# Kernel optimization log

Hardware: AMD Instinct MI355X
Metric: run time of the kernel (lower is better)

The kernel has to match this reference:

```python
import itertools
import jax, jax.numpy as jnp
import numpy as np

KERNEL = (2, 2)
NIN = 4            # prod(KERNEL)
NPAT = 16          # 2 ** NIN
# Faithful to the torch code: every kernel offset shifts dim 0 (the transposes
# swap dims 1 and d+1 and never touch dim 0), so each flattened kernel slot is a
# roll of x along axis 0 by -(sum of offsets), row-major over kernel indices.
SHIFTS = tuple(sum(idx) for idx in itertools.product(*(range(k) for k in KERNEL)))
BITS = np.asarray(list(itertools.product((0, 1), repeat=NIN)), dtype=np.float32)  # (NPAT, NIN)


def setup_inputs() -> dict:
    key = jax.random.key(0)
    k1, k2 = jax.random.split(key)
    x = jax.random.uniform(k1, (256, 64, 64), dtype=jnp.float32)                 # inputs in [0,1)
    toggle_gates = jax.random.uniform(k2, (4, NPAT, 64, 64), dtype=jnp.float32)  # torch.rand init
    return {"x": x, "toggle_gates": toggle_gates}


def _convolve(v):
    # (B,H,W) -> (B,H,W,NIN): shifted neighbor stack (rolls along dim 0, as in the torch code)
    return jnp.stack([jnp.roll(v, -s, axis=0) for s in SHIFTS], axis=-1)


def _pattern_weights(conv):
    # weight[b,h,w,p] = prod_j (conv_j if bit_j(p) else 1-conv_j)
    # equals prod_j (1 - |bit_j(p) - conv_j|) since bits are 0/1
    bits = jnp.asarray(BITS)  # (NPAT, NIN)
    w = jnp.ones(conv.shape[:-1] + (NPAT,), conv.dtype)
    for j in range(NIN):  # NIN=4, small fixed loop
        vj = conv[..., j:j + 1]  # (B,H,W,1)
        w = w * (vj * bits[:, j] + (1.0 - vj) * (1.0 - bits[:, j]))
    return w  # (B,H,W,NPAT)


def reference(x, toggle_gates):
    layers = toggle_gates.shape[0]
    tw = jax.nn.sigmoid(toggle_gates)  # (L,NPAT,H,W)
    outputs = x
    reg = jnp.asarray(0.0, x.dtype)
    for i in range(layers):
        conv = _convolve(outputs)          # (B,H,W,NIN)
        w = _pattern_weights(conv)         # (B,H,W,NPAT)
        if i:
            reg = reg - (jnp.mean(jnp.log(w)) + jnp.mean(jnp.log(1.0 - w)))
        # (weight * toggle).sum over pattern axis
        outputs = jnp.clip(jnp.einsum('bhwp,phw->bhw', w, tw[i]), 0.0, 1.0)
    return outputs, reg / (layers - 1)
```

## Files before the change

### kernel.cpp

```cpp
#include <hip/hip_runtime.h>

#define BATCH 256
#define HWSZ  4096
#define COLS  16
#define BSTR  17

__global__ __launch_bounds__(256) void fused_kernel(
    const float* __restrict__ x,
    const float* __restrict__ tg,
    float* __restrict__ out,
    float* __restrict__ partials)
{
    __shared__ float bufA[BATCH * BSTR];
    __shared__ float bufB[BATCH * BSTR];
    __shared__ float tws[64 * COLS];
    __shared__ float wsum[4];

    const int tid  = threadIdx.x;
    const int hw0  = blockIdx.x * COLS;
    const int c    = tid & 15;
    const int brow = tid >> 4;
    const int b0   = brow * 16;

#pragma unroll
    for (int k = 0; k < 4; ++k) {
        int idx = tid + k * 256;
        int c2 = idx & 15;
        int lp = idx >> 4;
        float g = tg[lp * HWSZ + hw0 + c2];
        tws[lp * COLS + c2] = 1.0f / (1.0f + __expf(-g));
    }

#pragma unroll
    for (int k = 0; k < 16; ++k) {
        int idx = tid + k * 256;
        int b = idx >> 4;
        int c2 = idx & 15;
        bufA[b * BSTR + c2] = x[b * HWSZ + hw0 + c2];
    }

    float racc = 0.0f;
    float* src = bufA;
    float* dst = bufB;

#pragma unroll
    for (int l = 0; l < 4; ++l) {
        __syncthreads();

        const float* tl = &tws[l * 16 * COLS + c];
        float T0  = tl[0 * COLS], T1 = tl[1 * COLS];
        float T24 = tl[2 * COLS] + tl[4 * COLS];
        float T35 = tl[3 * COLS] + tl[5 * COLS];
        float T6  = tl[6 * COLS], T7 = tl[7 * COLS];
        float T8  = tl[8 * COLS], T9 = tl[9 * COLS];
        float TAC = tl[10 * COLS] + tl[12 * COLS];
        float TBD = tl[11 * COLS] + tl[13 * COLS];
        float TE  = tl[14 * COLS], TF = tl[15 * COLS];

        float v0 = src[b0 * BSTR + c];
        float v1 = src[(b0 + 1) * BSTR + c];

#pragma unroll
        for (int k = 0; k < 16; ++k) {
            float v2 = src[((b0 + k + 2) & 255) * BSTR + c];
            float a0 = 1.0f - v0, a1 = 1.0f - v1, a2 = 1.0f - v2;

            float g0 = a1 * a1, g1 = a1 * v1, g2 = v1 * v1;
            float u00 = a0 * g0, u01 = a0 * g1, u02 = a0 * g2;
            float u10 = v0 * g0, u11 = v0 * g1, u12 = v0 * g2;

            float w0 = u00 * a2, w1 = u00 * v2;
            float w2 = u01 * a2, w3 = u01 * v2;
            float w6 = u02 * a2, w7 = u02 * v2;
            float w8 = u10 * a2, w9 = u10 * v2;
            float wA = u11 * a2, wB = u11 * v2;
            float wE = u12 * a2, wF = u12 * v2;

            float acc = w0 * T0 + w1 * T1 + w2 * T24 + w3 * T35
                      + w6 * T6 + w7 * T7 + w8 * T8 + w9 * T9
                      + wA * TAC + wB * TBD + wE * TE + wF * TF;
            float o = fminf(fmaxf(acc, 0.0f), 1.0f);

            if (l == 3) out[(b0 + k) * HWSZ + hw0 + c] = o;
            else        dst[(b0 + k) * BSTR + c] = o;

            if (l >= 1) {
                float s1 = (1.0f - w0) * (1.0f - w1) * (1.0f - w6) * (1.0f - w7)
                         * (1.0f - w8) * (1.0f - w9) * (1.0f - wE) * (1.0f - wF);
                float s2 = (1.0f - w2) * (1.0f - w3) * (1.0f - wA) * (1.0f - wB);
                float pB = s1 * s2 * s2;
                float pA = (v0 * a0) * (g1 * g1) * (v2 * a2);
                racc += 8.0f * __logf(pA) + __logf(pB);
            }
            v0 = v1; v1 = v2;
        }
        float* t = src; src = dst; dst = t;
    }

#pragma unroll
    for (int off = 32; off; off >>= 1) racc += __shfl_down(racc, off, 64);
    if ((tid & 63) == 0) wsum[tid >> 6] = racc;
    __syncthreads();
    if (tid == 0) partials[blockIdx.x] = wsum[0] + wsum[1] + wsum[2] + wsum[3];
}

__global__ void finalize_kernel(const float* __restrict__ partials,
                                float* __restrict__ out_reg)
{
    int tid = threadIdx.x;
    double v = (double)partials[tid];
#pragma unroll
    for (int off = 32; off; off >>= 1) v += __shfl_down(v, off, 64);
    __shared__ double ws[4];
    if ((tid & 63) == 0) ws[tid >> 6] = v;
    __syncthreads();
    if (tid == 0) {
        double tot = ws[0] + ws[1] + ws[2] + ws[3];
        out_reg[0] = (float)(-tot / (16777216.0 * 3.0));
    }
}

extern "C" void kernel_launch(void* const* d_in, const int* in_sizes, int n_in,
                              void* d_out, int out_size, void* d_ws, size_t ws_size,
                              hipStream_t stream)
{
    const float* x  = (const float*)d_in[0];
    const float* tg = (const float*)d_in[1];
    float* out      = (float*)d_out;
    float* partials = (float*)d_ws;

    fused_kernel<<<dim3(HWSZ / COLS), dim3(256), 0, stream>>>(x, tg, out, partials);
    finalize_kernel<<<1, 256, 0, stream>>>(partials, out + (size_t)BATCH * HWSZ);
}
```

Measured before the change: 72.48 us.

## Split batch across blocks with halo recompute to raise occupancy

Adds a second grid dimension that splits the batch into 64-row chunks. Each block loads an 8-row halo and recomputes the overlapping rows at each layer so the four layers still fuse without communicating between blocks. This shrinks shared memory per block and quadruples the block count, meant to fix low occupancy (256 blocks, ~35KB LDS each). The cost is redundant halo computation, extra loads, and four times as many partial sums for the finalize kernel.

After: 74.50 us. 1.03x slower.

```diff
diff --git a/kernel.cpp b/kernel.cpp
--- a/kernel.cpp
+++ b/kernel.cpp
@@ -4,23 +4,25 @@
 #define HWSZ  4096
 #define COLS  16
 #define BSTR  17
+#define CB    64
+#define XROWS (CB + 8)
 
-__global__ __launch_bounds__(256) void fused_kernel(
+__global__ __launch_bounds__(256, 4) void fused_kernel(
     const float* __restrict__ x,
     const float* __restrict__ tg,
     float* __restrict__ out,
     float* __restrict__ partials)
 {
-    __shared__ float bufA[BATCH * BSTR];
-    __shared__ float bufB[BATCH * BSTR];
+    __shared__ float bufA[XROWS * BSTR];
+    __shared__ float bufB[XROWS * BSTR];
     __shared__ float tws[64 * COLS];
     __shared__ float wsum[4];
 
-    const int tid  = threadIdx.x;
-    const int hw0  = blockIdx.x * COLS;
-    const int c    = tid & 15;
-    const int brow = tid >> 4;
-    const int b0   = brow * 16;
+    const int tid = threadIdx.x;
+    const int hw0 = blockIdx.x * COLS;
+    const int b0  = blockIdx.y * CB;
+    const int c   = tid & 15;
+    const int r   = tid >> 4;
 
 #pragma unroll
     for (int k = 0; k < 4; ++k) {
@@ -32,11 +34,13 @@
     }
 
 #pragma unroll
-    for (int k = 0; k < 16; ++k) {
+    for (int k = 0; k < 5; ++k) {
         int idx = tid + k * 256;
-        int b = idx >> 4;
-        int c2 = idx & 15;
-        bufA[b * BSTR + c2] = x[b * HWSZ + hw0 + c2];
+        if (idx < XROWS * COLS) {
+            int row = idx >> 4;
+            int c2  = idx & 15;
+            bufA[row * BSTR + c2] = x[((b0 + row) & 255) * HWSZ + hw0 + c2];
+        }
     }
 
     float racc = 0.0f;
@@ -45,6 +49,7 @@
 
 #pragma unroll
     for (int l = 0; l < 4; ++l) {
+        const int cnt = CB + 2 * (3 - l);
         __syncthreads();
 
         const float* tl = &tws[l * 16 * COLS + c];
@@ -57,42 +62,43 @@
         float TBD = tl[11 * COLS] + tl[13 * COLS];
         float TE  = tl[14 * COLS], TF = tl[15 * COLS];
 
-        float v0 = src[b0 * BSTR + c];
-        float v1 = src[(b0 + 1) * BSTR + c];
+#pragma unroll
+        for (int m = 0; m * 16 < CB + 2 * (3 - l); ++m) {
+            int idx = r + 16 * m;
+            if (idx < cnt) {
+                float v0 = src[idx * BSTR + c];
+                float v1 = src[(idx + 1) * BSTR + c];
+                float v2 = src[(idx + 2) * BSTR + c];
+                float a0 = 1.0f - v0, a1 = 1.0f - v1, a2 = 1.0f - v2;
 
-#pragma unroll
-        for (int k = 0; k < 16; ++k) {
-            float v2 = src[((b0 + k + 2) & 255) * BSTR + c];
-            float a0 = 1.0f - v0, a1 = 1.0f - v1, a2 = 1.0f - v2;
+                float g0 = a1 * a1, g1 = a1 * v1, g2 = v1 * v1;
+                float u00 = a0 * g0, u01 = a0 * g1, u02 = a0 * g2;
+                float u10 = v0 * g0, u11 = v0 * g1, u12 = v0 * g2;
 
-            float g0 = a1 * a1, g1 = a1 * v1, g2 = v1 * v1;
-            float u00 = a0 * g0, u01 = a0 * g1, u02 = a0 * g2;
-            float u10 = v0 * g0, u11 = v0 * g1, u12 = v0 * g2;
+                float w0 = u00 * a2, w1 = u00 * v2;
+                float w2 = u01 * a2, w3 = u01 * v2;
+                float w6 = u02 * a2, w7 = u02 * v2;
+                float w8 = u10 * a2, w9 = u10 * v2;
+                float wA = u11 * a2, wB = u11 * v2;
+                float wE = u12 * a2, wF = u12 * v2;
 
-            float w0 = u00 * a2, w1 = u00 * v2;
-            float w2 = u01 * a2, w3 = u01 * v2;
-            float w6 = u02 * a2, w7 = u02 * v2;
-            float w8 = u10 * a2, w9 = u10 * v2;
-            float wA = u11 * a2, wB = u11 * v2;
-            float wE = u12 * a2, wF = u12 * v2;
+                float acc = w0 * T0 + w1 * T1 + w2 * T24 + w3 * T35
+                          + w6 * T6 + w7 * T7 + w8 * T8 + w9 * T9
+                          + wA * TAC + wB * TBD + wE * TE + wF * TF;
+                float o = fminf(fmaxf(acc, 0.0f), 1.0f);
 
-            float acc = w0 * T0 + w1 * T1 + w2 * T24 + w3 * T35
-                      + w6 * T6 + w7 * T7 + w8 * T8 + w9 * T9
-                      + wA * TAC + wB * TBD + wE * TE + wF * TF;
-            float o = fminf(fmaxf(acc, 0.0f), 1.0f);
+                if (l == 3) out[(b0 + idx) * HWSZ + hw0 + c] = o;
+                else        dst[idx * BSTR + c] = o;
 
-            if (l == 3) out[(b0 + k) * HWSZ + hw0 + c] = o;
-            else        dst[(b0 + k) * BSTR + c] = o;
-
-            if (l >= 1) {
-                float s1 = (1.0f - w0) * (1.0f - w1) * (1.0f - w6) * (1.0f - w7)
-                         * (1.0f - w8) * (1.0f - w9) * (1.0f - wE) * (1.0f - wF);
-                float s2 = (1.0f - w2) * (1.0f - w3) * (1.0f - wA) * (1.0f - wB);
-                float pB = s1 * s2 * s2;
-                float pA = (v0 * a0) * (g1 * g1) * (v2 * a2);
-                racc += 8.0f * __logf(pA) + __logf(pB);
+                if (l >= 1 && idx < CB) {
+                    float s1 = (1.0f - w0) * (1.0f - w1) * (1.0f - w6) * (1.0f - w7)
+                             * (1.0f - w8) * (1.0f - w9) * (1.0f - wE) * (1.0f - wF);
+                    float s2 = (1.0f - w2) * (1.0f - w3) * (1.0f - wA) * (1.0f - wB);
+                    float pB = s1 * s2 * s2;
+                    float pA = (v0 * a0) * (g1 * g1) * (v2 * a2);
+                    racc += 8.0f * __logf(pA) + __logf(pB);
+                }
             }
-            v0 = v1; v1 = v2;
         }
         float* t = src; src = dst; dst = t;
     }
@@ -101,14 +107,18 @@
     for (int off = 32; off; off >>= 1) racc += __shfl_down(racc, off, 64);
     if ((tid & 63) == 0) wsum[tid >> 6] = racc;
     __syncthreads();
-    if (tid == 0) partials[blockIdx.x] = wsum[0] + wsum[1] + wsum[2] + wsum[3];
+    if (tid == 0)
+        partials[blockIdx.y * gridDim.x + blockIdx.x] =
+            wsum[0] + wsum[1] + wsum[2] + wsum[3];
 }
 
 __global__ void finalize_kernel(const float* __restrict__ partials,
                                 float* __restrict__ out_reg)
 {
     int tid = threadIdx.x;
-    double v = (double)partials[tid];
+    double v = 0.0;
+#pragma unroll
+    for (int k = 0; k < 4; ++k) v += (double)partials[tid + k * 256];
 #pragma unroll
     for (int off = 32; off; off >>= 1) v += __shfl_down(v, off, 64);
     __shared__ double ws[4];
@@ -129,6 +139,7 @@
     float* out      = (float*)d_out;
     float* partials = (float*)d_ws;
 
-    fused_kernel<<<dim3(HWSZ / COLS), dim3(256), 0, stream>>>(x, tg, out, partials);
+    fused_kernel<<<dim3(HWSZ / COLS, BATCH / CB), dim3(256), 0, stream>>>(
+        x, tg, out, partials);
     finalize_kernel<<<1, 256, 0, stream>>>(partials, out + (size_t)BATCH * HWSZ);
 }
```

## Hold batch rows in registers and pass neighbours by wave shuffles

Applied to the files above, without the earlier changes.

The kernel is restructured so each block handles 4 spatial columns with one wavefront per column. Each lane keeps 4 consecutive batch rows in registers and gets the next two rows from the neighbouring lane by shuffle, which replaces the per-layer shared-memory ping-pong buffers and the barriers between layers. This makes 1024 blocks with much less LDS each, raising occupancy, and loads and stores use float4 staged through a small shared transpose. The finalize kernel now sums 1024 partials.

Measured after the change: 76.00 us. 4.9% more time.

```diff
diff --git a/kernel.cpp b/kernel.cpp
--- a/kernel.cpp
+++ b/kernel.cpp
@@ -2,69 +2,59 @@
 
 #define BATCH 256
 #define HWSZ  4096
-#define COLS  16
-#define BSTR  17
 
-__global__ __launch_bounds__(256) void fused_kernel(
+__global__ __launch_bounds__(256, 4) void fused_kernel(
     const float* __restrict__ x,
     const float* __restrict__ tg,
     float* __restrict__ out,
     float* __restrict__ partials)
 {
-    __shared__ float bufA[BATCH * BSTR];
-    __shared__ float bufB[BATCH * BSTR];
-    __shared__ float tws[64 * COLS];
+    __shared__ float xs[BATCH * 5];
+    __shared__ float tws[256];
     __shared__ float wsum[4];
 
     const int tid  = threadIdx.x;
-    const int hw0  = blockIdx.x * COLS;
-    const int c    = tid & 15;
-    const int brow = tid >> 4;
-    const int b0   = brow * 16;
+    const int w    = tid >> 6;
+    const int lane = tid & 63;
+    const int nxt  = (lane + 1) & 63;
+    const int hw0  = blockIdx.x * 4;
 
-#pragma unroll
-    for (int k = 0; k < 4; ++k) {
-        int idx = tid + k * 256;
-        int c2 = idx & 15;
-        int lp = idx >> 4;
-        float g = tg[lp * HWSZ + hw0 + c2];
-        tws[lp * COLS + c2] = 1.0f / (1.0f + __expf(-g));
+    {
+        int lp = tid >> 2, cc = tid & 3;
+        float g = tg[lp * HWSZ + hw0 + cc];
+        tws[lp * 4 + cc] = 1.0f / (1.0f + __expf(-g));
     }
+    {
+        const float4 v = *reinterpret_cast<const float4*>(&x[tid * HWSZ + hw0]);
+        xs[tid * 5 + 0] = v.x; xs[tid * 5 + 1] = v.y;
+        xs[tid * 5 + 2] = v.z; xs[tid * 5 + 3] = v.w;
+    }
+    __syncthreads();
 
-#pragma unroll
-    for (int k = 0; k < 16; ++k) {
-        int idx = tid + k * 256;
-        int b = idx >> 4;
-        int c2 = idx & 15;
-        bufA[b * BSTR + c2] = x[b * HWSZ + hw0 + c2];
-    }
+    float cur0 = xs[(4 * lane + 0) * 5 + w];
+    float cur1 = xs[(4 * lane + 1) * 5 + w];
+    float cur2 = xs[(4 * lane + 2) * 5 + w];
+    float cur3 = xs[(4 * lane + 3) * 5 + w];
 
     float racc = 0.0f;
-    float* src = bufA;
-    float* dst = bufB;
 
 #pragma unroll
     for (int l = 0; l < 4; ++l) {
-        __syncthreads();
+        const float* tl = &tws[l * 64 + w];
+        float T0  = tl[0 * 4], T1 = tl[1 * 4];
+        float T24 = tl[2 * 4] + tl[4 * 4];
+        float T35 = tl[3 * 4] + tl[5 * 4];
+        float T6  = tl[6 * 4], T7 = tl[7 * 4];
+        float T8  = tl[8 * 4], T9 = tl[9 * 4];
+        float TAC = tl[10 * 4] + tl[12 * 4];
+        float TBD = tl[11 * 4] + tl[13 * 4];
+        float TE  = tl[14 * 4], TF = tl[15 * 4];
 
-        const float* tl = &tws[l * 16 * COLS + c];
-        float T0  = tl[0 * COLS], T1 = tl[1 * COLS];
-        float T24 = tl[2 * COLS] + tl[4 * COLS];
-        float T35 = tl[3 * COLS] + tl[5 * COLS];
-        float T6  = tl[6 * COLS], T7 = tl[7 * COLS];
-        float T8  = tl[8 * COLS], T9 = tl[9 * COLS];
-        float TAC = tl[10 * COLS] + tl[12 * COLS];
-        float TBD = tl[11 * COLS] + tl[13 * COLS];
-        float TE  = tl[14 * COLS], TF = tl[15 * COLS];
+        float e4 = __shfl(cur0, nxt, 64);
+        float e5 = __shfl(cur1, nxt, 64);
 
-        float v0 = src[b0 * BSTR + c];
-        float v1 = src[(b0 + 1) * BSTR + c];
-
-#pragma unroll
-        for (int k = 0; k < 16; ++k) {
-            float v2 = src[((b0 + k + 2) & 255) * BSTR + c];
+        auto elem = [&](float v0, float v1, float v2) -> float {
             float a0 = 1.0f - v0, a1 = 1.0f - v1, a2 = 1.0f - v2;
-
             float g0 = a1 * a1, g1 = a1 * v1, g2 = v1 * v1;
             float u00 = a0 * g0, u01 = a0 * g1, u02 = a0 * g2;
             float u10 = v0 * g0, u11 = v0 * g1, u12 = v0 * g2;
@@ -79,10 +69,6 @@
             float acc = w0 * T0 + w1 * T1 + w2 * T24 + w3 * T35
                       + w6 * T6 + w7 * T7 + w8 * T8 + w9 * T9
                       + wA * TAC + wB * TBD + wE * TE + wF * TF;
-            float o = fminf(fmaxf(acc, 0.0f), 1.0f);
-
-            if (l == 3) out[(b0 + k) * HWSZ + hw0 + c] = o;
-            else        dst[(b0 + k) * BSTR + c] = o;
 
             if (l >= 1) {
                 float s1 = (1.0f - w0) * (1.0f - w1) * (1.0f - w6) * (1.0f - w7)
@@ -92,23 +78,44 @@
                 float pA = (v0 * a0) * (g1 * g1) * (v2 * a2);
                 racc += 8.0f * __logf(pA) + __logf(pB);
             }
-            v0 = v1; v1 = v2;
-        }
-        float* t = src; src = dst; dst = t;
+            return fminf(fmaxf(acc, 0.0f), 1.0f);
+        };
+
+        float o0 = elem(cur0, cur1, cur2);
+        float o1 = elem(cur1, cur2, cur3);
+        float o2 = elem(cur2, cur3, e4);
+        float o3 = elem(cur3, e4, e5);
+        cur0 = o0; cur1 = o1; cur2 = o2; cur3 = o3;
+    }
+
+    __syncthreads();
+    xs[(4 * lane + 0) * 5 + w] = cur0;
+    xs[(4 * lane + 1) * 5 + w] = cur1;
+    xs[(4 * lane + 2) * 5 + w] = cur2;
+    xs[(4 * lane + 3) * 5 + w] = cur3;
+    __syncthreads();
+    {
+        float4 ov;
+        ov.x = xs[tid * 5 + 0]; ov.y = xs[tid * 5 + 1];
+        ov.z = xs[tid * 5 + 2]; ov.w = xs[tid * 5 + 3];
+        *reinterpret_cast<float4*>(&out[tid * HWSZ + hw0]) = ov;
     }
 
 #pragma unroll
     for (int off = 32; off; off >>= 1) racc += __shfl_down(racc, off, 64);
-    if ((tid & 63) == 0) wsum[tid >> 6] = racc;
+    if (lane == 0) wsum[w] = racc;
     __syncthreads();
-    if (tid == 0) partials[blockIdx.x] = wsum[0] + wsum[1] + wsum[2] + wsum[3];
+    if (tid == 0)
+        partials[blockIdx.x] = wsum[0] + wsum[1] + wsum[2] + wsum[3];
 }
 
 __global__ void finalize_kernel(const float* __restrict__ partials,
                                 float* __restrict__ out_reg)
 {
     int tid = threadIdx.x;
-    double v = (double)partials[tid];
+    double v = 0.0;
+#pragma unroll
+    for (int k = 0; k < 4; ++k) v += (double)partials[tid + k * 256];
 #pragma unroll
     for (int off = 32; off; off >>= 1) v += __shfl_down(v, off, 64);
     __shared__ double ws[4];
@@ -129,6 +136,6 @@
     float* out      = (float*)d_out;
     float* partials = (float*)d_ws;
 
-    fused_kernel<<<dim3(HWSZ / COLS), dim3(256), 0, stream>>>(x, tg, out, partials);
+    fused_kernel<<<dim3(HWSZ / 4), dim3(256), 0, stream>>>(x, tg, out, partials);
     finalize_kernel<<<1, 256, 0, stream>>>(partials, out + (size_t)BATCH * HWSZ);
 }
```
